# Kernel tuning notes

Hardware: AMD Instinct MI355X
Metric: run time of the kernel (lower is better)

## Reference

```python
import jax, jax.numpy as jnp
import numpy as np
import math

H = 16
D_MODEL = 1024
D_K = D_MODEL // H


def setup_inputs() -> dict:
    key0 = jax.random.key(0)
    ks = jax.random.split(key0, 20)
    B, S, D = 4, 1024, D_MODEL
    inp = {
        'query': jax.random.normal(ks[0], (B, S, D), jnp.float32),
        'key': jax.random.normal(ks[1], (B, S, D), jnp.float32),
        'value': jax.random.normal(ks[2], (B, S, D), jnp.float32),
        'mask': jnp.ones((B, 1, S), jnp.int32),
    }
    sc = 1.0 / math.sqrt(D)
    # linears[0]=key proj, [1]=value proj, [2]=query proj, [3]=output proj (per source)
    names = ['W_k', 'W_v', 'W_q', 'W_o', 'W_fq', 'W_fg']
    for i, n in enumerate(names):
        inp[n] = jax.random.normal(ks[3 + i], (D, D), jnp.float32) * sc
        inp['b' + n[1:]] = jnp.zeros((D,), jnp.float32)
    inp['up'] = jax.random.normal(ks[10], (H, 1, D_K), jnp.float32) * sc
    inp['uz'] = jax.random.normal(ks[11], (H, 1, D_K), jnp.float32) * sc
    return inp


def _heads(x, B, S):
    return jnp.transpose(x.reshape(B, S, H, D_K), (0, 2, 1, 3))  # [B,h,S,d_k]


def reference(query, key, value, mask, W_k, b_k, W_v, b_v, W_q, b_q, W_o, b_o, W_fq, b_fq, W_fg, b_fg, up, uz):
    B, S, D = query.shape
    k = _heads(key @ W_k.T + b_k, B, S)
    v = _heads(value @ W_v.T + b_v, B, S)
    q_lin = query @ W_q.T + b_q  # [B,S,D]
    # Gaussian focus bias
    glo = jnp.mean(q_lin, axis=1, keepdims=True)  # [B,1,D]
    c = jnp.tanh(q_lin @ W_fq.T + b_fq + (glo @ W_fg.T + b_fg))
    c = _heads(c, B, S)  # [B,h,S,d_k]
    p = jnp.sum(c * up, axis=-1)  # [B,h,S]
    z = jnp.sum(c * uz, axis=-1)
    P = jax.nn.sigmoid(p) * S
    Z = jax.nn.sigmoid(z) * S
    j = jnp.arange(S, dtype=P.dtype)  # key positions
    G = -((j[None, None, None, :] - P[..., None]) ** 2) * 2.0 / (Z[..., None] ** 2)  # [B,h,S,S]
    q = _heads(q_lin, B, S)
    scores = jnp.einsum('bhqd,bhkd->bhqk', q, k) / math.sqrt(D_K) + G
    scores = jnp.where(mask[:, None] == 0, jnp.float32(-1e15), scores)
    attn = jax.nn.softmax(scores, axis=-1)
    x = jnp.einsum('bhqk,bhkd->bhqd', attn, v)
    x = jnp.transpose(x, (0, 2, 1, 3)).reshape(B, S, D)
    out = x @ W_o.T + b_o
    return out, jnp.mean(attn, axis=1)
```

## Files before the change

### kernel.cpp

```cpp
#include <hip/hip_runtime.h>
#include <hip/hip_bf16.h>
#include <math.h>

typedef __attribute__((ext_vector_type(8))) short short8;
typedef __attribute__((ext_vector_type(4))) short short4v;
typedef __attribute__((ext_vector_type(4))) float f32x4;
typedef unsigned short u16;

#define SC2 0.18033688011112042f
#define L2E 1.4426950408889634f

__device__ __forceinline__ u16 f2bf(float f) {
  union { float f; unsigned u; } v; v.f = f;
  unsigned u = v.u + 0x7fffu + ((v.u >> 16) & 1u);
  return (u16)(u >> 16);
}
__device__ __forceinline__ float bf2f(u16 h) {
  union { unsigned u; float f; } v; v.u = ((unsigned)h) << 16;
  return v.f;
}
__device__ __forceinline__ float fexp2(float x) {
  float r; asm("v_exp_f32 %0, %1" : "=v"(r) : "v"(x)); return r;
}
__device__ __forceinline__ void gl_lds16(const u16* g, u16* l) {
  __builtin_amdgcn_global_load_lds(
      (const __attribute__((address_space(1))) void*)g,
      (__attribute__((address_space(3))) void*)l, 16, 0, 0);
}

__device__ __forceinline__ size_t KFoff(int b, int h, int j, int d) {
  return ((((size_t)(b * 16 + h) * 64 + (j >> 4)) * 2 + (d >> 5)) * 64
          + ((d >> 3) & 3) * 16 + (j & 15)) * 8 + (d & 7);
}
__device__ __forceinline__ size_t VFoff(int b, int h, int j, int d) {
  return ((((size_t)(b * 16 + h) * 4 + (d >> 4)) * 32 + (j >> 5)) * 64
          + ((j >> 3) & 3) * 16 + (d & 15)) * 8 + (j & 7);
}

__global__ __launch_bounds__(256) void cvt_all(
    const float* __restrict__ q, const float* __restrict__ k, const float* __restrict__ v,
    const float* __restrict__ w0, const float* __restrict__ w1, const float* __restrict__ w2,
    const float* __restrict__ w3, const float* __restrict__ w4,
    u16* __restrict__ qb, u16* __restrict__ kb, u16* __restrict__ vb,
    u16* __restrict__ w0b, u16* __restrict__ w1b, u16* __restrict__ w2b,
    u16* __restrict__ w3b, u16* __restrict__ w4b) {
  int bid = blockIdx.x;
  const float* s; u16* d; int base;
  if (bid < 2048)      { s = q; d = qb; base = bid; }
  else if (bid < 4096) { s = k; d = kb; base = bid - 2048; }
  else if (bid < 6144) { s = v; d = vb; base = bid - 4096; }
  else {
    int t2 = bid - 6144; int wi = t2 >> 9; base = t2 & 511;
    if (wi == 0)      { s = w0; d = w0b; }
    else if (wi == 1) { s = w1; d = w1b; }
    else if (wi == 2) { s = w2; d = w2b; }
    else if (wi == 3) { s = w3; d = w3b; }
    else              { s = w4; d = w4b; }
  }
  size_t idx = (size_t)base * 2048 + (size_t)threadIdx.x * 8;
  float4 a = *(const float4*)(s + idx);
  float4 b = *(const float4*)(s + idx + 4);
  short8 o;
  o[0] = (short)f2bf(a.x); o[1] = (short)f2bf(a.y); o[2] = (short)f2bf(a.z); o[3] = (short)f2bf(a.w);
  o[4] = (short)f2bf(b.x); o[5] = (short)f2bf(b.y); o[6] = (short)f2bf(b.z); o[7] = (short)f2bf(b.w);
  *(short8*)(d + idx) = o;
}

__global__ __launch_bounds__(256, 2)
void proj_qkv(const u16* __restrict__ qb, const u16* __restrict__ kb, const u16* __restrict__ vb,
              const u16* __restrict__ wqb, const u16* __restrict__ wkb, const u16* __restrict__ wvb,
              const float* __restrict__ bq, const float* __restrict__ bk, const float* __restrict__ bv,
              u16* __restrict__ Ql, u16* __restrict__ Kf, u16* __restrict__ Vf) {
  __shared__ u16 As[128 * 64];
  __shared__ u16 Bs[64 * 64];
  const int z = blockIdx.z;
  const u16* A  = (z == 0) ? kb : (z == 1) ? vb : qb;
  const u16* Bw = (z == 0) ? wkb : (z == 1) ? wvb : wqb;
  const float* bias = (z == 0) ? bk : (z == 1) ? bv : bq;
  const int tid = threadIdx.x;
  const int l = tid & 63, w = tid >> 6;
  const int m0 = blockIdx.x * 128, n0 = blockIdx.y * 64;
  const int wrow = (w & 1) * 64, wcol = (w >> 1) * 32;
  const int g = l >> 4, c = l & 15;

  f32x4 acc[4][2];
#pragma unroll
  for (int m = 0; m < 4; ++m)
#pragma unroll
    for (int n = 0; n < 2; ++n) acc[m][n] = (f32x4){0.f, 0.f, 0.f, 0.f};

  for (int k0 = 0; k0 < 1024; k0 += 64) {
#pragma unroll
    for (int p = 0; p < 4; ++p) {
      int idx = p * 256 + tid;
      int row = idx >> 3, slot = idx & 7;
      gl_lds16(A + (size_t)(m0 + row) * 1024 + k0 + ((slot ^ (row & 7)) * 8), As + idx * 8);
    }
#pragma unroll
    for (int p = 0; p < 2; ++p) {
      int idx = p * 256 + tid;
      int row = idx >> 3, slot = idx & 7;
      gl_lds16(Bw + (size_t)(n0 + row) * 1024 + k0 + ((slot ^ (row & 7)) * 8), Bs + idx * 8);
    }
    __syncthreads();
#pragma unroll
    for (int kk = 0; kk < 2; ++kk) {
      short8 af[4], bf[2];
#pragma unroll
      for (int m = 0; m < 4; ++m) {
        int row = wrow + m * 16 + c;
        af[m] = *(const short8*)(As + row * 64 + (((kk * 4 + g) ^ (row & 7)) * 8));
      }
#pragma unroll
      for (int n = 0; n < 2; ++n) {
        int row = wcol + n * 16 + c;
        bf[n] = *(const short8*)(Bs + row * 64 + (((kk * 4 + g) ^ (row & 7)) * 8));
      }
#pragma unroll
      for (int m = 0; m < 4; ++m)
#pragma unroll
        for (int n = 0; n < 2; ++n)
          acc[m][n] = __builtin_amdgcn_mfma_f32_16x16x32_bf16(af[m], bf[n], acc[m][n], 0, 0, 0);
    }
    __syncthreads();
  }

#pragma unroll
  for (int n = 0; n < 2; ++n) {
    int col = n0 + wcol + n * 16 + c;
    float bv_ = bias[col];
    int hh = col >> 6, dd = col & 63;
#pragma unroll
    for (int m = 0; m < 4; ++m) {
#pragma unroll
      for (int r = 0; r < 4; ++r) {
        int rowg = m0 + wrow + m * 16 + g * 4 + r;
        float val = acc[m][n][r] + bv_;
        int bb = rowg >> 10, jj = rowg & 1023;
        if (z == 0)      Kf[KFoff(bb, hh, jj, dd)] = f2bf(val);
        else if (z == 1) Vf[VFoff(bb, hh, jj, dd)] = f2bf(val);
        else             Ql[(size_t)rowg * 1024 + col] = f2bf(val);
      }
    }
  }
}

template<int EPI>
__global__ __launch_bounds__(256, 2)
void gemm_bt(const u16* __restrict__ A, const u16* __restrict__ Bw,
             const float* __restrict__ bias, const float* __restrict__ gb,
             void* __restrict__ Cout) {
  __shared__ u16 As[128 * 64];
  __shared__ u16 Bs[64 * 64];
  const int tid = threadIdx.x;
  const int l = tid & 63, w = tid >> 6;
  const int m0 = blockIdx.x * 128, n0 = blockIdx.y * 64;
  const int wrow = (w & 1) * 64, wcol = (w >> 1) * 32;
  const int g = l >> 4, c = l & 15;

  f32x4 acc[4][2];
#pragma unroll
  for (int m = 0; m < 4; ++m)
#pragma unroll
    for (int n = 0; n < 2; ++n) acc[m][n] = (f32x4){0.f, 0.f, 0.f, 0.f};

  for (int k0 = 0; k0 < 1024; k0 += 64) {
#pragma unroll
    for (int p = 0; p < 4; ++p) {
      int idx = p * 256 + tid;
      int row = idx >> 3, slot = idx & 7;
      gl_lds16(A + (size_t)(m0 + row) * 1024 + k0 + ((slot ^ (row & 7)) * 8), As + idx * 8);
    }
#pragma unroll
    for (int p = 0; p < 2; ++p) {
      int idx = p * 256 + tid;
      int row = idx >> 3, slot = idx & 7;
      gl_lds16(Bw + (size_t)(n0 + row) * 1024 + k0 + ((slot ^ (row & 7)) * 8), Bs + idx * 8);
    }
    __syncthreads();
#pragma unroll
    for (int kk = 0; kk < 2; ++kk) {
      short8 af[4], bf[2];
#pragma unroll
      for (int m = 0; m < 4; ++m) {
        int row = wrow + m * 16 + c;
        af[m] = *(const short8*)(As + row * 64 + (((kk * 4 + g) ^ (row & 7)) * 8));
      }
#pragma unroll
      for (int n = 0; n < 2; ++n) {
        int row = wcol + n * 16 + c;
        bf[n] = *(const short8*)(Bs + row * 64 + (((kk * 4 + g) ^ (row & 7)) * 8));
      }
#pragma unroll
      for (int m = 0; m < 4; ++m)
#pragma unroll
        for (int n = 0; n < 2; ++n)
          acc[m][n] = __builtin_amdgcn_mfma_f32_16x16x32_bf16(af[m], bf[n], acc[m][n], 0, 0, 0);
    }
    __syncthreads();
  }

#pragma unroll
  for (int n = 0; n < 2; ++n) {
    int col = n0 + wcol + n * 16 + c;
    float bv;
    if (EPI == 1) bv = gb[(m0 >> 10) * 1024 + col];
    else bv = bias[col];
#pragma unroll
    for (int m = 0; m < 4; ++m) {
#pragma unroll
      for (int r = 0; r < 4; ++r) {
        int rowg = m0 + wrow + m * 16 + g * 4 + r;
        float val = acc[m][n][r] + bv;
        if (EPI == 1) val = tanhf(val);
        if (EPI == 2) ((float*)Cout)[(size_t)rowg * 1024 + col] = val;
        else ((u16*)Cout)[(size_t)rowg * 1024 + col] = f2bf(val);
      }
    }
  }
}

__global__ __launch_bounds__(128) void glo_part_k(const u16* __restrict__ qlin, float* __restrict__ gpart) {
  int b = blockIdx.x & 3, seg = blockIdx.x >> 2;
  int t = threadIdx.x;
  float acc[8] = {0, 0, 0, 0, 0, 0, 0, 0};
  for (int s = seg * 16; s < seg * 16 + 16; ++s) {
    short8 v = *(const short8*)(qlin + (size_t)(b * 1024 + s) * 1024 + t * 8);
#pragma unroll
    for (int j = 0; j < 8; ++j) acc[j] += bf2f((u16)v[j]);
  }
#pragma unroll
  for (int j = 0; j < 8; ++j) gpart[(size_t)(seg * 4 + b) * 1024 + t * 8 + j] = acc[j];
}

__global__ __launch_bounds__(128) void glo_reduce(const float* __restrict__ gpart, float* __restrict__ glo) {
  int b = blockIdx.x & 3, cc = blockIdx.x >> 2;
  int col = cc * 128 + threadIdx.x;
  float a[8] = {0, 0, 0, 0, 0, 0, 0, 0};
#pragma unroll
  for (int s8 = 0; s8 < 8; ++s8) {
#pragma unroll
    for (int s = 0; s < 8; ++s)
      a[s] += gpart[(size_t)((s8 * 8 + s) * 4 + b) * 1024 + col];
  }
  float t = ((a[0] + a[1]) + (a[2] + a[3])) + ((a[4] + a[5]) + (a[6] + a[7]));
  glo[b * 1024 + col] = t * (1.0f / 1024.0f);
}

__global__ __launch_bounds__(256) void gbias_k(const float* __restrict__ glo, const float* __restrict__ Wfg,
                                               const float* __restrict__ bfq, const float* __restrict__ bfg,
                                               float* __restrict__ gbias) {
  __shared__ float glo_l[4096];
  int tid = threadIdx.x;
  for (int idx = tid; idx < 4096; idx += 256) glo_l[idx] = glo[idx];
  __syncthreads();
  int w = tid >> 6, l = tid & 63;
#pragma unroll
  for (int i = 0; i < 4; ++i) {
    int n = blockIdx.x * 16 + w * 4 + i;
    float a0 = 0, a1 = 0, a2 = 0, a3 = 0;
#pragma unroll
    for (int kk = 0; kk < 4; ++kk) {
      int k = kk * 256 + l * 4;
      float4 wv = *(const float4*)(Wfg + (size_t)n * 1024 + k);
      float4 g0 = *(const float4*)(&glo_l[k]);
      float4 g1 = *(const float4*)(&glo_l[1024 + k]);
      float4 g2 = *(const float4*)(&glo_l[2048 + k]);
      float4 g3 = *(const float4*)(&glo_l[3072 + k]);
      a0 += wv.x * g0.x + wv.y * g0.y + wv.z * g0.z + wv.w * g0.w;
      a1 += wv.x * g1.x + wv.y * g1.y + wv.z * g1.z + wv.w * g1.w;
      a2 += wv.x * g2.x + wv.y * g2.y + wv.z * g2.z + wv.w * g2.w;
      a3 += wv.x * g3.x + wv.y * g3.y + wv.z * g3.z + wv.w * g3.w;
    }
#pragma unroll
    for (int d = 1; d < 64; d <<= 1) {
      a0 += __shfl_xor(a0, d); a1 += __shfl_xor(a1, d);
      a2 += __shfl_xor(a2, d); a3 += __shfl_xor(a3, d);
    }
    if (l == 0) {
      float bb = bfq[n] + bfg[n];
      gbias[n] = a0 + bb; gbias[1024 + n] = a1 + bb;
      gbias[2048 + n] = a2 + bb; gbias[3072 + n] = a3 + bb;
    }
  }
}

__global__ __launch_bounds__(256) void pz_kernel(const u16* __restrict__ cbuf,
                                                 const float* __restrict__ up, const float* __restrict__ uz,
                                                 float* __restrict__ Pout, float* __restrict__ IZout) {
  __shared__ float lup[1024], luz[1024];
  int tid = threadIdx.x;
  for (int i = tid; i < 1024; i += 256) { lup[i] = up[i]; luz[i] = uz[i]; }
  __syncthreads();
  int w = tid >> 6, l = tid & 63;
  int sg = blockIdx.x * 4 + w;
  int b = sg >> 10, s = sg & 1023;
  const u16* crow = cbuf + (size_t)sg * 1024;
  for (int h = 0; h < 16; ++h) {
    float cv = bf2f(crow[h * 64 + l]);
    float pp = cv * lup[h * 64 + l];
    float zz = cv * luz[h * 64 + l];
#pragma unroll
    for (int d = 1; d < 64; d <<= 1) { pp += __shfl_xor(pp, d); zz += __shfl_xor(zz, d); }
    if (l == 0) {
      float Pv = 1024.f / (1.f + __expf(-pp));
      float Zv = 1024.f / (1.f + __expf(-zz));
      size_t o = (size_t)(b * 16 + h) * 1024 + s;
      Pout[o] = Pv;
      IZout[o] = 2.0f / (Zv * Zv) * L2E;
    }
  }
}

template<int WP>
__global__ __launch_bounds__(512, 4)
void attn_flash(const u16* __restrict__ Qlin, const u16* __restrict__ Kf, const u16* __restrict__ Vf,
                const float* __restrict__ Pbuf, const float* __restrict__ IZbuf,
                const int* __restrict__ mask,
                u16* __restrict__ xbuf, float* __restrict__ Mbuf, float* __restrict__ iLbuf,
                u16* __restrict__ Pall, float* __restrict__ mch) {
  __shared__ u16 sm16[24576];
  __shared__ float maskb_s[1024];

  const int tid = threadIdx.x;
  const int l = tid & 63, w = tid >> 6;
  const int g = l >> 4, c = l & 15;
  const int bid = blockIdx.x;
  const int bh = (bid & 7) + ((bid >> 6) << 3);
  const int qc = (bid >> 3) & 7;
  const int b = bh >> 4, h = bh & 15;
  const int q0w = qc * 128 + w * 16;

  char* ps_ = (char*)(sm16 + 16384) + w * 2048;

  const u16* KfH = Kf + (size_t)bh * 65536;
  const u16* VfH = Vf + (size_t)bh * 65536;
  const int sdt = tid >> 7, sinner = tid & 127;

#pragma unroll
  for (int i = 0; i < 2; ++i) {
    int idx = i * 512 + tid;
    maskb_s[idx] = (mask[b * 1024 + idx] == 0) ? -1.4e15f : 0.0f;
  }

  const u16* qrow = Qlin + (size_t)(b * 1024 + q0w + c) * 1024 + h * 64 + g * 8;
  short8 af0 = *(const short8*)qrow;
  short8 af1 = *(const short8*)(qrow + 32);
  float Pq[4], IZq[4];
#pragma unroll
  for (int r = 0; r < 4; ++r) {
    size_t o = (size_t)bh * 1024 + q0w + g * 4 + r;
    Pq[r] = Pbuf[o]; IZq[r] = IZbuf[o];
  }

  float m[4], lsum[4];
  f32x4 xacc[4];
#pragma unroll
  for (int r = 0; r < 4; ++r) { m[r] = -3.0e38f; lsum[r] = 0.f; }
#pragma unroll
  for (int dt = 0; dt < 4; ++dt) xacc[dt] = (f32x4){0.f, 0.f, 0.f, 0.f};

  gl_lds16(KfH + (size_t)0 * 4096 + tid * 8, sm16 + tid * 8);
  gl_lds16(VfH + ((size_t)(sdt * 32 + 0) * 512) + sinner * 8, sm16 + 4096 + tid * 8);
  __syncthreads();

  for (int jc = 0; jc < 16; ++jc) {
    const int bi = jc & 1;
    u16* Ksb = sm16 + bi * 8192;
    u16* Vsb = Ksb + 4096;
    if (jc < 15) {
      u16* Ksn = sm16 + (bi ^ 1) * 8192;
      gl_lds16(KfH + (size_t)(jc + 1) * 4096 + tid * 8, Ksn + tid * 8);
      gl_lds16(VfH + ((size_t)(sdt * 32 + (jc + 1) * 2) * 512) + sinner * 8, Ksn + 4096 + tid * 8);
    }

    f32x4 sc[4];
    float cm[4] = {-3.0e38f, -3.0e38f, -3.0e38f, -3.0e38f};
#pragma unroll
    for (int t = 0; t < 4; ++t) {
      short8 b0 = *(const short8*)(Ksb + (t * 2 + 0) * 512 + l * 8);
      short8 b1 = *(const short8*)(Ksb + (t * 2 + 1) * 512 + l * 8);
      f32x4 z = (f32x4){0.f, 0.f, 0.f, 0.f};
      z = __builtin_amdgcn_mfma_f32_16x16x32_bf16(af0, b0, z, 0, 0, 0);
      z = __builtin_amdgcn_mfma_f32_16x16x32_bf16(af1, b1, z, 0, 0, 0);
      int j = jc * 64 + t * 16 + c;
      float jf = (float)j, mbv = maskb_s[j];
#pragma unroll
      for (int r = 0; r < 4; ++r) {
        float diff = jf - Pq[r];
        float s = z[r] * SC2 + mbv - diff * diff * IZq[r];
        sc[t][r] = s;
        cm[r] = fmaxf(cm[r], s);
      }
    }
#pragma unroll
    for (int d = 1; d < 16; d <<= 1)
#pragma unroll
      for (int r = 0; r < 4; ++r) cm[r] = fmaxf(cm[r], __shfl_xor(cm[r], d));
    float scale[4], ps[4];
#pragma unroll
    for (int r = 0; r < 4; ++r) {
      float nm = fmaxf(m[r], cm[r]);
      scale[r] = fexp2(m[r] - nm);
      m[r] = nm;
      ps[r] = 0.f;
    }
#pragma unroll
    for (int t = 0; t < 4; ++t) {
#pragma unroll
      for (int r = 0; r < 4; ++r) {
        float p = fexp2(sc[t][r] - m[r]);
        ps[r] += p;
        int row = g * 4 + r;
        int byte = (row * 128 + (t * 16 + c) * 2) ^ ((row & 7) << 4);
        *(u16*)(ps_ + byte) = f2bf(p);
      }
    }
#pragma unroll
    for (int r = 0; r < 4; ++r) {
      lsum[r] = lsum[r] * scale[r] + ps[r];
#pragma unroll
      for (int dt = 0; dt < 4; ++dt) xacc[dt][r] *= scale[r];
    }
    if (WP && c == 0) {
#pragma unroll
      for (int r = 0; r < 4; ++r)
        mch[((size_t)bh * 16 + jc) * 1024 + q0w + g * 4 + r] = m[r];
    }
    if (WP) {
#pragma unroll
      for (int k2 = 0; k2 < 2; ++k2) {
        int i = k2 * 512 + l * 8;
        int row = i >> 6, col = i & 63;
        int byte = (row * 128 + col * 2) ^ ((row & 7) << 4);
        short8 v = *(const short8*)(ps_ + byte);
        *(short8*)(Pall + (((size_t)bh * 16 + jc) * 1024 + q0w + row) * 64 + col) = v;
      }
    }
    short8 pa[2];
#pragma unroll
    for (int ks = 0; ks < 2; ++ks) {
      int abyte = (c * 128 + (ks * 32 + g * 8) * 2) ^ ((c & 7) << 4);
      pa[ks] = *(const short8*)(ps_ + abyte);
    }
#pragma unroll
    for (int dt = 0; dt < 4; ++dt) {
#pragma unroll
      for (int ks = 0; ks < 2; ++ks) {
        short8 vb = *(const short8*)(Vsb + (dt * 2 + ks) * 512 + l * 8);
        xacc[dt] = __builtin_amdgcn_mfma_f32_16x16x32_bf16(pa[ks], vb, xacc[dt], 0, 0, 0);
      }
    }
    __syncthreads();
  }

#pragma unroll
  for (int d = 1; d < 16; d <<= 1)
#pragma unroll
    for (int r = 0; r < 4; ++r) lsum[r] += __shfl_xor(lsum[r], d);
  float iLr[4];
#pragma unroll
  for (int r = 0; r < 4; ++r) iLr[r] = 1.0f / lsum[r];
  if (c == 0) {
#pragma unroll
    for (int r = 0; r < 4; ++r) {
      size_t o = (size_t)bh * 1024 + q0w + g * 4 + r;
      Mbuf[o] = m[r];
      iLbuf[o] = iLr[r];
    }
  }
  float* xs = (float*)sm16 + w * 1024;
#pragma unroll
  for (int dt = 0; dt < 4; ++dt)
#pragma unroll
    for (int r = 0; r < 4; ++r)
      xs[(g * 4 + r) * 64 + dt * 16 + c] = xacc[dt][r] * iLr[r];
#pragma unroll
  for (int k2 = 0; k2 < 4; ++k2) {
    int i = k2 * 256 + l * 4;
    int row = i >> 6, d0 = i & 63;
    f32x4 xv = *(const f32x4*)(xs + i);
    short4v o;
    o[0] = (short)f2bf(xv.x); o[1] = (short)f2bf(xv.y);
    o[2] = (short)f2bf(xv.z); o[3] = (short)f2bf(xv.w);
    *(short4v*)(xbuf + (size_t)(b * 1024 + q0w + row) * 1024 + h * 64 + d0) = o;
  }
}

__global__ __launch_bounds__(256, 2)
void epilogue_k(const u16* __restrict__ A, const u16* __restrict__ Bw,
                const float* __restrict__ bias, float* __restrict__ out0,
                const u16* __restrict__ Pall, const float* __restrict__ iLbuf,
                const float* __restrict__ Mbuf, const float* __restrict__ mchb,
                float* __restrict__ out2, int usePall) {
  __shared__ u16 As[128 * 64];
  __shared__ u16 Bs[64 * 64];
  const int bid = blockIdx.x;
  const int tid = threadIdx.x;
  if (bid >= 512) {
    if (!usePall) return;
    int bq = (bid - 512) * 2 + (tid >> 7);
    int b = bq >> 10, q = bq & 1023;
    int j = (tid & 127) * 8;
    int jc = j >> 6, jin = j & 63;
    float acc[8] = {0, 0, 0, 0, 0, 0, 0, 0};
    for (int h = 0; h < 16; ++h) {
      int bh = b * 16 + h;
      float M = Mbuf[(size_t)bh * 1024 + q];
      float iLh = iLbuf[(size_t)bh * 1024 + q];
      float mc = mchb[((size_t)bh * 16 + jc) * 1024 + q];
      float f = fexp2(mc - M) * iLh;
      short8 p = *(const short8*)(Pall + (((size_t)bh * 16 + jc) * 1024 + q) * 64 + jin);
#pragma unroll
      for (int i = 0; i < 8; ++i) acc[i] = fmaf(bf2f((u16)p[i]), f, acc[i]);
    }
    float* dst = out2 + (size_t)bq * 1024 + j;
#pragma unroll
    for (int i = 0; i < 8; ++i) dst[i] = acc[i] * 0.0625f;
    return;
  }
  const int l = tid & 63, w = tid >> 6;
  const int m0 = (bid & 31) * 128, n0 = (bid >> 5) * 64;
  const int wrow = (w & 1) * 64, wcol = (w >> 1) * 32;
  const int g = l >> 4, c = l & 15;

  f32x4 acc[4][2];
#pragma unroll
  for (int m = 0; m < 4; ++m)
#pragma unroll
    for (int n = 0; n < 2; ++n) acc[m][n] = (f32x4){0.f, 0.f, 0.f, 0.f};

  for (int k0 = 0; k0 < 1024; k0 += 64) {
#pragma unroll
    for (int p = 0; p < 4; ++p) {
      int idx = p * 256 + tid;
      int row = idx >> 3, slot = idx & 7;
      gl_lds16(A + (size_t)(m0 + row) * 1024 + k0 + ((slot ^ (row & 7)) * 8), As + idx * 8);
    }
#pragma unroll
    for (int p = 0; p < 2; ++p) {
      int idx = p * 256 + tid;
      int row = idx >> 3, slot = idx & 7;
      gl_lds16(Bw + (size_t)(n0 + row) * 1024 + k0 + ((slot ^ (row & 7)) * 8), Bs + idx * 8);
    }
    __syncthreads();
#pragma unroll
    for (int kk = 0; kk < 2; ++kk) {
      short8 af[4], bf[2];
#pragma unroll
      for (int m = 0; m < 4; ++m) {
        int row = wrow + m * 16 + c;
        af[m] = *(const short8*)(As + row * 64 + (((kk * 4 + g) ^ (row & 7)) * 8));
      }
#pragma unroll
      for (int n = 0; n < 2; ++n) {
        int row = wcol + n * 16 + c;
        bf[n] = *(const short8*)(Bs + row * 64 + (((kk * 4 + g) ^ (row & 7)) * 8));
      }
#pragma unroll
      for (int m = 0; m < 4; ++m)
#pragma unroll
        for (int n = 0; n < 2; ++n)
          acc[m][n] = __builtin_amdgcn_mfma_f32_16x16x32_bf16(af[m], bf[n], acc[m][n], 0, 0, 0);
    }
    __syncthreads();
  }
#pragma unroll
  for (int n = 0; n < 2; ++n) {
    int col = n0 + wcol + n * 16 + c;
    float bv = bias[col];
#pragma unroll
    for (int m = 0; m < 4; ++m) {
#pragma unroll
      for (int r = 0; r < 4; ++r) {
        int rowg = m0 + wrow + m * 16 + g * 4 + r;
        out0[(size_t)rowg * 1024 + col] = acc[m][n][r] + bv;
      }
    }
  }
}

__global__ __launch_bounds__(512, 4)
void attn_mean(const u16* __restrict__ Qlin, const u16* __restrict__ Kf,
               const float* __restrict__ Pbuf, const float* __restrict__ IZbuf,
               const float* __restrict__ Mbuf, const float* __restrict__ iLbuf,
               const int* __restrict__ mask,
               float* __restrict__ out2) {
  const int tid = threadIdx.x;
  const int l = tid & 63, w = tid >> 6;
  const int g = l >> 4, c = l & 15;
  int chunk = (blockIdx.x % 8) * 64 + blockIdx.x / 8;
  const int b = chunk >> 7;
  const int qt = (chunk & 127) >> 1;
  const int jh = chunk & 1;
  const int q0 = qt * 16;
  const int jbase = jh * 512 + w * 64;

  float mb[4];
#pragma unroll
  for (int t = 0; t < 4; ++t)
    mb[t] = (mask[b * 1024 + jbase + t * 16 + c] == 0) ? -1.4e15f : 0.0f;

  f32x4 macc[4];
#pragma unroll
  for (int t = 0; t < 4; ++t) macc[t] = (f32x4){0.f, 0.f, 0.f, 0.f};

  for (int h = 0; h < 16; ++h) {
    const u16* qrow = Qlin + (size_t)(b * 1024 + q0 + c) * 1024 + h * 64 + g * 8;
    short8 af0 = *(const short8*)qrow;
    short8 af1 = *(const short8*)(qrow + 32);
    const u16* kb2 = Kf + ((size_t)((b * 16 + h) * 64 + jh * 32 + w * 4) * 2) * 512 + l * 8;
    float Pq[4], IZq[4], Mq[4], iLq[4];
#pragma unroll
    for (int r = 0; r < 4; ++r) {
      size_t o = (size_t)(b * 16 + h) * 1024 + q0 + g * 4 + r;
      Pq[r] = Pbuf[o]; IZq[r] = IZbuf[o]; Mq[r] = Mbuf[o]; iLq[r] = iLbuf[o] * 0.0625f;
    }
#pragma unroll
    for (int t = 0; t < 4; ++t) {
      short8 bf0 = *(const short8*)(kb2 + t * 1024);
      short8 bf1 = *(const short8*)(kb2 + t * 1024 + 512);
      f32x4 z = (f32x4){0.f, 0.f, 0.f, 0.f};
      z = __builtin_amdgcn_mfma_f32_16x16x32_bf16(af0, bf0, z, 0, 0, 0);
      z = __builtin_amdgcn_mfma_f32_16x16x32_bf16(af1, bf1, z, 0, 0, 0);
      float jf = (float)(jbase + t * 16 + c);
#pragma unroll
      for (int r = 0; r < 4; ++r) {
        float diff = jf - Pq[r];
        float s = z[r] * SC2 + mb[t] - diff * diff * IZq[r];
        macc[t][r] += fexp2(s - Mq[r]) * iLq[r];
      }
    }
  }
#pragma unroll
  for (int t = 0; t < 4; ++t) {
#pragma unroll
    for (int r = 0; r < 4; ++r)
      out2[(size_t)(b * 1024 + q0 + g * 4 + r) * 1024 + jbase + t * 16 + c] = macc[t][r];
  }
}

extern "C" void kernel_launch(void* const* d_in, const int* in_sizes, int n_in,
                              void* d_out, int out_size, void* d_ws, size_t ws_size,
                              hipStream_t stream) {
  const float* q   = (const float*)d_in[0];
  const float* k   = (const float*)d_in[1];
  const float* v   = (const float*)d_in[2];
  const int*   msk = (const int*)d_in[3];
  const float* Wk  = (const float*)d_in[4];  const float* bk  = (const float*)d_in[5];
  const float* Wv  = (const float*)d_in[6];  const float* bv  = (const float*)d_in[7];
  const float* Wq  = (const float*)d_in[8];  const float* bq  = (const float*)d_in[9];
  const float* Wo  = (const float*)d_in[10]; const float* bo  = (const float*)d_in[11];
  const float* Wfq = (const float*)d_in[12]; const float* bfq = (const float*)d_in[13];
  const float* Wfg = (const float*)d_in[14]; const float* bfg = (const float*)d_in[15];
  const float* up  = (const float*)d_in[16]; const float* uz  = (const float*)d_in[17];

  const size_t MB = 1u << 20;
  char* base = (char*)d_ws;
  char* p = base;
  auto take = [&](size_t n) { char* r = p; p += (n + 255) & ~(size_t)255; return r; };
  u16* Kf   = (u16*)take(8 * MB);
  u16* Ql   = (u16*)take(8 * MB);
  u16* Vf   = (u16*)take(8 * MB);
  u16* xb   = (u16*)take(8 * MB);
  u16* wob  = (u16*)take(2 * MB);
  float* Pb    = (float*)take((size_t)65536 * 4);
  float* IZb   = (float*)take((size_t)65536 * 4);
  float* Mb    = (float*)take((size_t)65536 * 4);
  float* iLb   = (float*)take((size_t)65536 * 4);
  float* mch   = (float*)take((size_t)64 * 16 * 1024 * 4);
  float* gpart = (float*)take((size_t)64 * 4 * 1024 * 4);
  float* glo   = (float*)take(4096 * 4);
  float* gbias = (float*)take(4096 * 4);
  size_t pool_off = (size_t)(p - base);
  u16* qb   = (u16*)take(8 * MB);
  u16* kb   = (u16*)take(8 * MB);
  u16* vb   = (u16*)take(8 * MB);
  u16* wkb  = (u16*)take(2 * MB);
  u16* wvb  = (u16*)take(2 * MB);
  u16* wqb  = (u16*)take(2 * MB);
  u16* wfqb = (u16*)take(2 * MB);
  u16* Cc   = (u16*)take(8 * MB);
  u16* Pall = (u16*)(base + pool_off);
  int usePall = (ws_size >= pool_off + (size_t)128 * MB) ? 1 : 0;

  float* out0 = (float*)d_out;
  float* out2 = out0 + (size_t)4 * 1024 * 1024;

  cvt_all<<<8704, 256, 0, stream>>>(q, k, v, Wk, Wv, Wq, Wfq, Wo,
                                    qb, kb, vb, wkb, wvb, wqb, wfqb, wob);
  dim3 gg3(32, 16, 3);
  proj_qkv<<<gg3, 256, 0, stream>>>(qb, kb, vb, wqb, wkb, wvb, bq, bk, bv, Ql, Kf, Vf);
  dim3 gg(32, 16);
  glo_part_k<<<256, 128, 0, stream>>>(Ql, gpart);
  glo_reduce<<<32, 128, 0, stream>>>(gpart, glo);
  gbias_k<<<64, 256, 0, stream>>>(glo, Wfg, bfq, bfg, gbias);
  gemm_bt<1><<<gg, 256, 0, stream>>>(Ql, wfqb, nullptr, gbias, Cc);
  pz_kernel<<<1024, 256, 0, stream>>>(Cc, up, uz, Pb, IZb);
  if (usePall) {
    attn_flash<1><<<512, 512, 0, stream>>>(Ql, Kf, Vf, Pb, IZb, msk, xb, Mb, iLb, Pall, mch);
    epilogue_k<<<2560, 256, 0, stream>>>(xb, wob, bo, out0, Pall, iLb, Mb, mch, out2, 1);
  } else {
    attn_flash<0><<<512, 512, 0, stream>>>(Ql, Kf, Vf, Pb, IZb, msk, xb, Mb, iLb, Pall, mch);
    attn_mean<<<512, 512, 0, stream>>>(Ql, Kf, Pb, IZb, Mb, iLb, msk, out2);
    epilogue_k<<<512, 256, 0, stream>>>(xb, wob, bo, out0, Pall, iLb, Mb, mch, out2, 0);
  }
}
```

Before: 200.2 us.

## Widen GEMM tiles to 128x128 and skip flash rescale when max unchanged

```diff
diff --git a/kernel.cpp b/kernel.cpp
--- a/kernel.cpp
+++ b/kernel.cpp
@@ -66,67 +66,61 @@
   *(short8*)(d + idx) = o;
 }
 
+#define GEMM_CORE(A_, Bw_)                                                              \
+  f32x4 acc[4][4];                                                                      \
+  _Pragma("unroll") for (int m = 0; m < 4; ++m)                                         \
+    _Pragma("unroll") for (int n = 0; n < 4; ++n)                                       \
+      acc[m][n] = (f32x4){0.f, 0.f, 0.f, 0.f};                                          \
+  for (int k0 = 0; k0 < 1024; k0 += 64) {                                               \
+    _Pragma("unroll") for (int p = 0; p < 4; ++p) {                                     \
+      int idx = p * 256 + tid;                                                          \
+      int row = idx >> 3, slot = idx & 7;                                               \
+      gl_lds16(A_ + (size_t)(m0 + row) * 1024 + k0 + ((slot ^ (row & 7)) * 8), As + idx * 8); \
+    }                                                                                   \
+    _Pragma("unroll") for (int p = 0; p < 4; ++p) {                                     \
+      int idx = p * 256 + tid;                                                          \
+      int row = idx >> 3, slot = idx & 7;                                               \
+      gl_lds16(Bw_ + (size_t)(n0 + row) * 1024 + k0 + ((slot ^ (row & 7)) * 8), Bs + idx * 8); \
+    }                                                                                   \
+    __syncthreads();                                                                    \
+    _Pragma("unroll") for (int kk = 0; kk < 2; ++kk) {                                  \
+      short8 af[4], bf[4];                                                              \
+      _Pragma("unroll") for (int m = 0; m < 4; ++m) {                                   \
+        int row = wrow + m * 16 + c;                                                    \
+        af[m] = *(const short8*)(As + row * 64 + (((kk * 4 + g) ^ (row & 7)) * 8));     \
+      }                                                                                 \
+      _Pragma("unroll") for (int n = 0; n < 4; ++n) {                                   \
+        int row = wcol + n * 16 + c;                                                    \
+        bf[n] = *(const short8*)(Bs + row * 64 + (((kk * 4 + g) ^ (row & 7)) * 8));     \
+      }                                                                                 \
+      _Pragma("unroll") for (int m = 0; m < 4; ++m)                                     \
+        _Pragma("unroll") for (int n = 0; n < 4; ++n)                                   \
+          acc[m][n] = __builtin_amdgcn_mfma_f32_16x16x32_bf16(af[m], bf[n], acc[m][n], 0, 0, 0); \
+    }                                                                                   \
+    __syncthreads();                                                                    \
+  }
+
 __global__ __launch_bounds__(256, 2)
 void proj_qkv(const u16* __restrict__ qb, const u16* __restrict__ kb, const u16* __restrict__ vb,
               const u16* __restrict__ wqb, const u16* __restrict__ wkb, const u16* __restrict__ wvb,
               const float* __restrict__ bq, const float* __restrict__ bk, const float* __restrict__ bv,
               u16* __restrict__ Ql, u16* __restrict__ Kf, u16* __restrict__ Vf) {
   __shared__ u16 As[128 * 64];
-  __shared__ u16 Bs[64 * 64];
+  __shared__ u16 Bs[128 * 64];
   const int z = blockIdx.z;
   const u16* A  = (z == 0) ? kb : (z == 1) ? vb : qb;
   const u16* Bw = (z == 0) ? wkb : (z == 1) ? wvb : wqb;
   const float* bias = (z == 0) ? bk : (z == 1) ? bv : bq;
   const int tid = threadIdx.x;
   const int l = tid & 63, w = tid >> 6;
-  const int m0 = blockIdx.x * 128, n0 = blockIdx.y * 64;
-  const int wrow = (w & 1) * 64, wcol = (w >> 1) * 32;
+  const int m0 = blockIdx.x * 128, n0 = blockIdx.y * 128;
+  const int wrow = (w & 1) * 64, wcol = (w >> 1) * 64;
   const int g = l >> 4, c = l & 15;
 
-  f32x4 acc[4][2];
-#pragma unroll
-  for (int m = 0; m < 4; ++m)
-#pragma unroll
-    for (int n = 0; n < 2; ++n) acc[m][n] = (f32x4){0.f, 0.f, 0.f, 0.f};
-
-  for (int k0 = 0; k0 < 1024; k0 += 64) {
-#pragma unroll
-    for (int p = 0; p < 4; ++p) {
-      int idx = p * 256 + tid;
-      int row = idx >> 3, slot = idx & 7;
-      gl_lds16(A + (size_t)(m0 + row) * 1024 + k0 + ((slot ^ (row & 7)) * 8), As + idx * 8);
-    }
-#pragma unroll
-    for (int p = 0; p < 2; ++p) {
-      int idx = p * 256 + tid;
-      int row = idx >> 3, slot = idx & 7;
-      gl_lds16(Bw + (size_t)(n0 + row) * 1024 + k0 + ((slot ^ (row & 7)) * 8), Bs + idx * 8);
-    }
-    __syncthreads();
-#pragma unroll
-    for (int kk = 0; kk < 2; ++kk) {
-      short8 af[4], bf[2];
-#pragma unroll
-      for (int m = 0; m < 4; ++m) {
-        int row = wrow + m * 16 + c;
-        af[m] = *(const short8*)(As + row * 64 + (((kk * 4 + g) ^ (row & 7)) * 8));
-      }
-#pragma unroll
-      for (int n = 0; n < 2; ++n) {
-        int row = wcol + n * 16 + c;
-        bf[n] = *(const short8*)(Bs + row * 64 + (((kk * 4 + g) ^ (row & 7)) * 8));
-      }
-#pragma unroll
-      for (int m = 0; m < 4; ++m)
-#pragma unroll
-        for (int n = 0; n < 2; ++n)
-          acc[m][n] = __builtin_amdgcn_mfma_f32_16x16x32_bf16(af[m], bf[n], acc[m][n], 0, 0, 0);
-    }
-    __syncthreads();
-  }
-
-#pragma unroll
-  for (int n = 0; n < 2; ++n) {
+  GEMM_CORE(A, Bw)
+
+#pragma unroll
+  for (int n = 0; n < 4; ++n) {
     int col = n0 + wcol + n * 16 + c;
     float bv_ = bias[col];
     int hh = col >> 6, dd = col & 63;
@@ -145,76 +139,29 @@
   }
 }
 
-template<int EPI>
 __global__ __launch_bounds__(256, 2)
-void gemm_bt(const u16* __restrict__ A, const u16* __restrict__ Bw,
-             const float* __restrict__ bias, const float* __restrict__ gb,
-             void* __restrict__ Cout) {
+void gemm_tanh(const u16* __restrict__ A, const u16* __restrict__ Bw,
+               const float* __restrict__ gb, u16* __restrict__ Cout) {
   __shared__ u16 As[128 * 64];
-  __shared__ u16 Bs[64 * 64];
+  __shared__ u16 Bs[128 * 64];
   const int tid = threadIdx.x;
   const int l = tid & 63, w = tid >> 6;
-  const int m0 = blockIdx.x * 128, n0 = blockIdx.y * 64;
-  const int wrow = (w & 1) * 64, wcol = (w >> 1) * 32;
+  const int m0 = blockIdx.x * 128, n0 = blockIdx.y * 128;
+  const int wrow = (w & 1) * 64, wcol = (w >> 1) * 64;
   const int g = l >> 4, c = l & 15;
 
-  f32x4 acc[4][2];
-#pragma unroll
-  for (int m = 0; m < 4; ++m)
-#pragma unroll
-    for (int n = 0; n < 2; ++n) acc[m][n] = (f32x4){0.f, 0.f, 0.f, 0.f};
-
-  for (int k0 = 0; k0 < 1024; k0 += 64) {
-#pragma unroll
-    for (int p = 0; p < 4; ++p) {
-      int idx = p * 256 + tid;
-      int row = idx >> 3, slot = idx & 7;
-      gl_lds16(A + (size_t)(m0 + row) * 1024 + k0 + ((slot ^ (row & 7)) * 8), As + idx * 8);
-    }
-#pragma unroll
-    for (int p = 0; p < 2; ++p) {
-      int idx = p * 256 + tid;
-      int row = idx >> 3, slot = idx & 7;
-      gl_lds16(Bw + (size_t)(n0 + row) * 1024 + k0 + ((slot ^ (row & 7)) * 8), Bs + idx * 8);
-    }
-    __syncthreads();
-#pragma unroll
-    for (int kk = 0; kk < 2; ++kk) {
-      short8 af[4], bf[2];
-#pragma unroll
-      for (int m = 0; m < 4; ++m) {
-        int row = wrow + m * 16 + c;
-        af[m] = *(const short8*)(As + row * 64 + (((kk * 4 + g) ^ (row & 7)) * 8));
-      }
-#pragma unroll
-      for (int n = 0; n < 2; ++n) {
-        int row = wcol + n * 16 + c;
-        bf[n] = *(const short8*)(Bs + row * 64 + (((kk * 4 + g) ^ (row & 7)) * 8));
-      }
-#pragma unroll
-      for (int m = 0; m < 4; ++m)
-#pragma unroll
-        for (int n = 0; n < 2; ++n)
-          acc[m][n] = __builtin_amdgcn_mfma_f32_16x16x32_bf16(af[m], bf[n], acc[m][n], 0, 0, 0);
-    }
-    __syncthreads();
-  }
-
-#pragma unroll
-  for (int n = 0; n < 2; ++n) {
+  GEMM_CORE(A, Bw)
+
+#pragma unroll
+  for (int n = 0; n < 4; ++n) {
     int col = n0 + wcol + n * 16 + c;
-    float bv;
-    if (EPI == 1) bv = gb[(m0 >> 10) * 1024 + col];
-    else bv = bias[col];
+    float bv = gb[(m0 >> 10) * 1024 + col];
 #pragma unroll
     for (int m = 0; m < 4; ++m) {
 #pragma unroll
       for (int r = 0; r < 4; ++r) {
         int rowg = m0 + wrow + m * 16 + g * 4 + r;
-        float val = acc[m][n][r] + bv;
-        if (EPI == 1) val = tanhf(val);
-        if (EPI == 2) ((float*)Cout)[(size_t)rowg * 1024 + col] = val;
-        else ((u16*)Cout)[(size_t)rowg * 1024 + col] = f2bf(val);
+        Cout[(size_t)rowg * 1024 + col] = f2bf(tanhf(acc[m][n][r] + bv));
       }
     }
   }
@@ -397,14 +344,19 @@
     for (int d = 1; d < 16; d <<= 1)
 #pragma unroll
       for (int r = 0; r < 4; ++r) cm[r] = fmaxf(cm[r], __shfl_xor(cm[r], d));
+    bool grow = (cm[0] > m[0]) | (cm[1] > m[1]) | (cm[2] > m[2]) | (cm[3] > m[3]);
+    const bool resc = __any(grow);
     float scale[4], ps[4];
-#pragma unroll
-    for (int r = 0; r < 4; ++r) {
-      float nm = fmaxf(m[r], cm[r]);
-      scale[r] = fexp2(m[r] - nm);
-      m[r] = nm;
-      ps[r] = 0.f;
-    }
+    if (resc) {
+#pragma unroll
+      for (int r = 0; r < 4; ++r) {
+        float nm = fmaxf(m[r], cm[r]);
+        scale[r] = fexp2(m[r] - nm);
+        m[r] = nm;
+      }
+    }
+#pragma unroll
+    for (int r = 0; r < 4; ++r) ps[r] = 0.f;
 #pragma unroll
     for (int t = 0; t < 4; ++t) {
 #pragma unroll
@@ -416,11 +368,16 @@
         *(u16*)(ps_ + byte) = f2bf(p);
       }
     }
-#pragma unroll
-    for (int r = 0; r < 4; ++r) {
-      lsum[r] = lsum[r] * scale[r] + ps[r];
-#pragma unroll
-      for (int dt = 0; dt < 4; ++dt) xacc[dt][r] *= scale[r];
+    if (resc) {
+#pragma unroll
+      for (int r = 0; r < 4; ++r) {
+        lsum[r] = lsum[r] * scale[r] + ps[r];
+#pragma unroll
+        for (int dt = 0; dt < 4; ++dt) xacc[dt][r] *= scale[r];
+      }
+    } else {
+#pragma unroll
+      for (int r = 0; r < 4; ++r) lsum[r] += ps[r];
     }
     if (WP && c == 0) {
 #pragma unroll
@@ -494,12 +451,12 @@
                 const float* __restrict__ Mbuf, const float* __restrict__ mchb,
                 float* __restrict__ out2, int usePall) {
   __shared__ u16 As[128 * 64];
-  __shared__ u16 Bs[64 * 64];
+  __shared__ u16 Bs[128 * 64];
   const int bid = blockIdx.x;
   const int tid = threadIdx.x;
-  if (bid >= 512) {
+  if (bid >= 256) {
     if (!usePall) return;
-    int bq = (bid - 512) * 2 + (tid >> 7);
+    int bq = (bid - 256) * 2 + (tid >> 7);
     int b = bq >> 10, q = bq & 1023;
     int j = (tid & 127) * 8;
     int jc = j >> 6, jin = j & 63;
@@ -520,53 +477,14 @@
     return;
   }
   const int l = tid & 63, w = tid >> 6;
-  const int m0 = (bid & 31) * 128, n0 = (bid >> 5) * 64;
-  const int wrow = (w & 1) * 64, wcol = (w >> 1) * 32;
+  const int m0 = (bid & 31) * 128, n0 = (bid >> 5) * 128;
+  const int wrow = (w & 1) * 64, wcol = (w >> 1) * 64;
   const int g = l >> 4, c = l & 15;
 
-  f32x4 acc[4][2];
-#pragma unroll
-  for (int m = 0; m < 4; ++m)
-#pragma unroll
-    for (int n = 0; n < 2; ++n) acc[m][n] = (f32x4){0.f, 0.f, 0.f, 0.f};
-
-  for (int k0 = 0; k0 < 1024; k0 += 64) {
-#pragma unroll
-    for (int p = 0; p < 4; ++p) {
-      int idx = p * 256 + tid;
-      int row = idx >> 3, slot = idx & 7;
-      gl_lds16(A + (size_t)(m0 + row) * 1024 + k0 + ((slot ^ (row & 7)) * 8), As + idx * 8);
-    }
-#pragma unroll
-    for (int p = 0; p < 2; ++p) {
-      int idx = p * 256 + tid;
-      int row = idx >> 3, slot = idx & 7;
-      gl_lds16(Bw + (size_t)(n0 + row) * 1024 + k0 + ((slot ^ (row & 7)) * 8), Bs + idx * 8);
-    }
-    __syncthreads();
-#pragma unroll
-    for (int kk = 0; kk < 2; ++kk) {
-      short8 af[4], bf[2];
-#pragma unroll
-      for (int m = 0; m < 4; ++m) {
-        int row = wrow + m * 16 + c;
-        af[m] = *(const short8*)(As + row * 64 + (((kk * 4 + g) ^ (row & 7)) * 8));
-      }
-#pragma unroll
-      for (int n = 0; n < 2; ++n) {
-        int row = wcol + n * 16 + c;
-        bf[n] = *(const short8*)(Bs + row * 64 + (((kk * 4 + g) ^ (row & 7)) * 8));
-      }
-#pragma unroll
-      for (int m = 0; m < 4; ++m)
-#pragma unroll
-        for (int n = 0; n < 2; ++n)
-          acc[m][n] = __builtin_amdgcn_mfma_f32_16x16x32_bf16(af[m], bf[n], acc[m][n], 0, 0, 0);
-    }
-    __syncthreads();
-  }
-#pragma unroll
-  for (int n = 0; n < 2; ++n) {
+  GEMM_CORE(A, Bw)
+
+#pragma unroll
+  for (int n = 0; n < 4; ++n) {
     int col = n0 + wcol + n * 16 + c;
     float bv = bias[col];
 #pragma unroll
@@ -689,20 +607,20 @@
 
   cvt_all<<<8704, 256, 0, stream>>>(q, k, v, Wk, Wv, Wq, Wfq, Wo,
                                     qb, kb, vb, wkb, wvb, wqb, wfqb, wob);
-  dim3 gg3(32, 16, 3);
+  dim3 gg3(32, 8, 3);
   proj_qkv<<<gg3, 256, 0, stream>>>(qb, kb, vb, wqb, wkb, wvb, bq, bk, bv, Ql, Kf, Vf);
-  dim3 gg(32, 16);
+  dim3 gg(32, 8);
   glo_part_k<<<256, 128, 0, stream>>>(Ql, gpart);
   glo_reduce<<<32, 128, 0, stream>>>(gpart, glo);
   gbias_k<<<64, 256, 0, stream>>>(glo, Wfg, bfq, bfg, gbias);
-  gemm_bt<1><<<gg, 256, 0, stream>>>(Ql, wfqb, nullptr, gbias, Cc);
+  gemm_tanh<<<gg, 256, 0, stream>>>(Ql, wfqb, gbias, Cc);
   pz_kernel<<<1024, 256, 0, stream>>>(Cc, up, uz, Pb, IZb);
   if (usePall) {
     attn_flash<1><<<512, 512, 0, stream>>>(Ql, Kf, Vf, Pb, IZb, msk, xb, Mb, iLb, Pall, mch);
-    epilogue_k<<<2560, 256, 0, stream>>>(xb, wob, bo, out0, Pall, iLb, Mb, mch, out2, 1);
+    epilogue_k<<<2304, 256, 0, stream>>>(xb, wob, bo, out0, Pall, iLb, Mb, mch, out2, 1);
   } else {
     attn_flash<0><<<512, 512, 0, stream>>>(Ql, Kf, Vf, Pb, IZb, msk, xb, Mb, iLb, Pall, mch);
     attn_mean<<<512, 512, 0, stream>>>(Ql, Kf, Pb, IZb, Mb, iLb, msk, out2);
-    epilogue_k<<<512, 256, 0, stream>>>(xb, wob, bo, out0, Pall, iLb, Mb, mch, out2, 0);
-  }
-}
+    epilogue_k<<<256, 256, 0, stream>>>(xb, wob, bo, out0, Pall, iLb, Mb, mch, out2, 0);
+  }
+}
```

New measurement: 202.2 us. No clear change (+1.0%).
